# Kernel tuning notes

Measured on AMD Instinct MI355X. Metric: run time of the kernel, lower is better.

Reference implementation:

```python
import jax, jax.numpy as jnp
import numpy as np

N, F_IN, HID, HEADS, E, G, CLS = 20000, 128, 32, 8, 320000, 64, 10


def setup_inputs() -> dict:
    key = jax.random.key(0)
    ks = jax.random.split(key, 16)
    HC = HEADS * HID
    inp = {
        'x': jax.random.normal(ks[0], (N, F_IN), jnp.float32),
        'edge_index': jax.random.randint(ks[1], (2, E), 0, N, jnp.int64),
        'batch': jnp.sort(jax.random.randint(ks[2], (N,), 0, G, jnp.int64)),
        'W1': jax.random.normal(ks[3], (F_IN, HC), jnp.float32) * 0.1,
        'att_l1': jax.random.normal(ks[4], (HEADS, HID), jnp.float32) * 0.1,
        'att_r1': jax.random.normal(ks[5], (HEADS, HID), jnp.float32) * 0.1,
        'b1': jnp.zeros((HC,), jnp.float32),
        'W2': jax.random.normal(ks[6], (HC, HC), jnp.float32) * 0.1,
        'att_l2': jax.random.normal(ks[7], (HEADS, HID), jnp.float32) * 0.1,
        'att_r2': jax.random.normal(ks[8], (HEADS, HID), jnp.float32) * 0.1,
        'b2': jnp.zeros((HC,), jnp.float32),
        'lin_W': jax.random.normal(ks[9], (HC, CLS), jnp.float32) * 0.1,
        'lin_b': jnp.zeros((CLS,), jnp.float32),
    }
    return inp


def _add_self_loops(edge_index):
    loops = jnp.arange(N, dtype=edge_index.dtype)
    return (jnp.concatenate([edge_index[0], loops]),
            jnp.concatenate([edge_index[1], loops]))


def _supergat_conv(x, edge_index, W, att_l, att_r, b):
    # SuperGATConv, attention_type='MX', eval mode (no dropout / neg sampling)
    h = (x @ W).reshape(-1, HEADS, HID)          # [N, H, C]
    src, dst = _add_self_loops(edge_index)       # j -> i
    x_j = h[src]                                 # [Etot, H, C]
    x_i = h[dst]
    logits = jnp.einsum('ehc,ehc->eh', x_i, x_j)            # dot-product part
    alpha = jnp.einsum('ehc,hc->eh', x_j, att_l) + jnp.einsum('ehc,hc->eh', x_i, att_r)
    alpha = alpha * jax.nn.sigmoid(logits)
    alpha = jax.nn.leaky_relu(alpha, 0.2)
    # segment softmax over incoming edges of each dst node
    amax = jax.ops.segment_max(alpha, dst, num_segments=N)
    ex = jnp.exp(alpha - amax[dst])
    denom = jax.ops.segment_sum(ex, dst, num_segments=N)
    attn = ex / (denom[dst] + 1e-16)             # [Etot, H]
    out = jax.ops.segment_sum(x_j * attn[..., None], dst, num_segments=N)  # [N,H,C]
    return out.reshape(-1, HEADS * HID) + b


def reference(x, edge_index, batch, W1, att_l1, att_r1, b1, W2, att_l2, att_r2, b2, lin_W, lin_b):
    h = _supergat_conv(x, edge_index, W1, att_l1, att_r1, b1)
    h = jax.nn.elu(h)
    h = _supergat_conv(h, edge_index, W2, att_l2, att_r2, b2)
    # global mean pool over graphs
    sums = jax.ops.segment_sum(h, batch, num_segments=G)
    cnts = jax.ops.segment_sum(jnp.ones((h.shape[0], 1), h.dtype), batch, num_segments=G)
    pooled = sums / jnp.maximum(cnts, 1.0)
    return pooled @ lin_W + lin_b
```

## Files before the change

### kernel.cpp

```cpp
#include <hip/hip_runtime.h>
#include <hip/hip_bf16.h>
#include <math.h>

#define NNODE 20000
#define FIN   128
#define HC    256
#define HEADS 8
#define HID   32
#define NEDGE 320000
#define ETOT  (NEDGE + NNODE)
#define NGRAPH 64
#define NCLS  10
#define MAXDEG 64

typedef __attribute__((ext_vector_type(8))) short short8v;
typedef __attribute__((ext_vector_type(8))) unsigned short ushort8v;
typedef __attribute__((ext_vector_type(4))) float float4v;

__device__ __forceinline__ ushort f2bf(float f) {
    __hip_bfloat16 b = __float2bfloat16(f);
    return *(ushort*)&b;
}
__device__ __forceinline__ float bf2f(ushort u) {
    return __uint_as_float(((unsigned)u) << 16);
}


#define ZB_DEG ((NNODE + 255) / 256)
#define ZB_PS  ((NGRAPH * HC + NGRAPH + 255) / 256)

__global__ __launch_bounds__(256) void init_kernel(const float* __restrict__ W1,
                                                   const float* __restrict__ W2,
                                                   ushort* __restrict__ W1t,
                                                   ushort* __restrict__ W2t,
                                                   int* __restrict__ deg,
                                                   float* __restrict__ psum) {
    int b = blockIdx.x;
    if (b < 128) {
        int e = b * 256 + threadIdx.x;
        int k = e >> 8, n = e & 255;
        W1t[(long)n * FIN + k] = f2bf(W1[(long)k * 256 + n]);
    } else if (b < 384) {
        int e = (b - 128) * 256 + threadIdx.x;
        int k = e >> 8, n = e & 255;
        W2t[(long)n * HC + k] = f2bf(W2[(long)k * 256 + n]);
    } else if (b < 384 + ZB_DEG) {
        int i = (b - 384) * 256 + threadIdx.x;
        if (i < NNODE) deg[i] = 0;
    } else {
        int i = (b - 384 - ZB_DEG) * 256 + threadIdx.x;
        if (i < NGRAPH * HC + NGRAPH) psum[i] = 0.f;
    }
}


__global__ __launch_bounds__(256) void fill_slots(const int* __restrict__ ei,
                                                  int* __restrict__ deg,
                                                  int* __restrict__ esrc) {
    int e = blockIdx.x * blockDim.x + threadIdx.x;
    if (e >= ETOT) return;
    int src, dst;
    if (e < NEDGE) { src = ei[e]; dst = ei[NEDGE + e]; }
    else           { src = e - NEDGE; dst = src; }
    int slot = atomicAdd(&deg[dst], 1);
    if (slot < MAXDEG) esrc[dst * MAXDEG + slot] = src;
}


template<bool A_FP32>
__global__ __launch_bounds__(256) void gemm_mfma(const void* __restrict__ Aptr,
                                                 const ushort* __restrict__ Bt,
                                                 ushort* __restrict__ C,
                                                 const float* __restrict__ attL,
                                                 const float* __restrict__ attR,
                                                 float* __restrict__ aL,
                                                 float* __restrict__ aR,
                                                 int M, int K) {
    __shared__ __align__(16) ushort As[64][72];
    __shared__ __align__(16) ushort Bs[64][72];
    int tid = threadIdx.x;
    int rowBase = blockIdx.x * 64;
    int colBase = blockIdx.y * 64;
    int wave = tid >> 6;
    int l = tid & 63;
    int lm = l & 15;
    int quad = l >> 4;
    int r0 = (wave >> 1) * 32;
    int c0 = (wave & 1) * 32;

    float4v acc00 = {0.f, 0.f, 0.f, 0.f};
    float4v acc01 = acc00, acc10 = acc00, acc11 = acc00;

    for (int k0 = 0; k0 < K; k0 += 64) {
        if (A_FP32) {
            const float* A = (const float*)Aptr;
            #pragma unroll
            for (int q = 0; q < 4; q++) {
                int idx = tid + q * 256;
                int r   = idx >> 4;
                int kc  = (idx & 15) * 4;
                int grow = rowBase + r;
                float4 v = make_float4(0.f, 0.f, 0.f, 0.f);
                if (grow < M) v = *(const float4*)(A + (long)grow * K + k0 + kc);
                ushort4 o = { f2bf(v.x), f2bf(v.y), f2bf(v.z), f2bf(v.w) };
                *(ushort4*)&As[r][kc] = o;
            }
            #pragma unroll
            for (int q = 0; q < 2; q++) {
                int ch = tid + q * 256;
                int r  = ch >> 3;
                int kc = (ch & 7) * 8;
                *(short8v*)&Bs[r][kc] =
                    *(const short8v*)(Bt + (long)(colBase + r) * K + k0 + kc);
            }
        } else {
            const ushort* A = (const ushort*)Aptr;
            #pragma unroll
            for (int q = 0; q < 2; q++) {
                int ch = tid + q * 256;
                int r  = ch >> 3;
                int kc = (ch & 7) * 8;
                int grow = rowBase + r;
                short8v av = {};
                if (grow < M) av = *(const short8v*)(A + (long)grow * K + k0 + kc);
                *(short8v*)&As[r][kc] = av;
                *(short8v*)&Bs[r][kc] =
                    *(const short8v*)(Bt + (long)(colBase + r) * K + k0 + kc);
            }
        }
        __syncthreads();
        #pragma unroll
        for (int ks = 0; ks < 64; ks += 32) {
            int kb = ks + quad * 8;
            short8v a0 = *(const short8v*)&As[r0 + lm][kb];
            short8v a1 = *(const short8v*)&As[r0 + 16 + lm][kb];
            short8v b0 = *(const short8v*)&Bs[c0 + lm][kb];
            short8v b1 = *(const short8v*)&Bs[c0 + 16 + lm][kb];
            acc00 = __builtin_amdgcn_mfma_f32_16x16x32_bf16(a0, b0, acc00, 0, 0, 0);
            acc01 = __builtin_amdgcn_mfma_f32_16x16x32_bf16(a0, b1, acc01, 0, 0, 0);
            acc10 = __builtin_amdgcn_mfma_f32_16x16x32_bf16(a1, b0, acc10, 0, 0, 0);
            acc11 = __builtin_amdgcn_mfma_f32_16x16x32_bf16(a1, b1, acc11, 0, 0, 0);
        }
        __syncthreads();
    }

    int cb = colBase + c0;
    int hd = cb >> 5;
    float al0 = attL[cb + lm], al1 = attL[cb + 16 + lm];
    float ar0 = attR[cb + lm], ar1 = attR[cb + 16 + lm];
    #pragma unroll
    for (int mi = 0; mi < 2; mi++) {
        float4v s0 = mi ? acc10 : acc00;
        float4v s1 = mi ? acc11 : acc01;
        #pragma unroll
        for (int r = 0; r < 4; r++) {
            int row = rowBase + r0 + mi * 16 + quad * 4 + r;
            float pl = s0[r] * al0 + s1[r] * al1;
            float pr = s0[r] * ar0 + s1[r] * ar1;
            #pragma unroll
            for (int s2 = 1; s2 < 16; s2 <<= 1) {
                pl += __shfl_xor(pl, s2);
                pr += __shfl_xor(pr, s2);
            }
            if (row < M) {
                C[(long)row * 256 + cb + lm]      = f2bf(s0[r]);
                C[(long)row * 256 + cb + 16 + lm] = f2bf(s1[r]);
                if (lm == 0) {
                    aL[row * 8 + hd] = pl;
                    aR[row * 8 + hd] = pr;
                }
            }
        }
    }
}


__global__ __launch_bounds__(256) void fused_attn(const ushort* __restrict__ h,
                                                  const int* __restrict__ degv,
                                                  const int* __restrict__ esrc,
                                                  const float* __restrict__ aL,
                                                  const float* __restrict__ aR,
                                                  const float* __restrict__ bias,
                                                  ushort* __restrict__ out,
                                                  int apply_elu) {
    int wave = threadIdx.x >> 6;
    int node = blockIdx.x * 4 + wave;
    if (node >= NNODE) return;
    int l = threadIdx.x & 63;
    int slot = l >> 5;
    int lh = l & 31;
    int head = lh >> 2;

    const ushort8v* h8 = (const ushort8v*)h;
    ushort8v hiu = h8[(long)node * 32 + lh];
    float hi[8];
    #pragma unroll
    for (int c = 0; c < 8; c++) hi[c] = bf2f(hiu[c]);
    float a_ri = aR[node * 8 + head];
    int beg = node * MAXDEG;
    int deg = min(degv[node], MAXDEG);

    float lsum = 0.f;
    float acc[8] = {0.f, 0.f, 0.f, 0.f, 0.f, 0.f, 0.f, 0.f};

    int p  = slot;
    int j  = (p < deg)     ? esrc[beg + p]     : 0;
    int jn = (p + 2 < deg) ? esrc[beg + p + 2] : 0;
    for (; p < deg; p += 2) {
        ushort8v hju = h8[(long)j * 32 + lh];
        float a_lj = aL[j * 8 + head];
        j = jn;
        jn = (p + 4 < deg) ? esrc[beg + p + 4] : 0;
        float hj[8];
        #pragma unroll
        for (int c = 0; c < 8; c++) hj[c] = bf2f(hju[c]);
        float prod = hi[0] * hj[0];
        #pragma unroll
        for (int c = 1; c < 8; c++) prod += hi[c] * hj[c];
        prod += __shfl_xor(prod, 1);
        prod += __shfl_xor(prod, 2);
        float alpha = (a_lj + a_ri) * __builtin_amdgcn_rcpf(1.f + __expf(-prod));
        alpha = (alpha > 0.f) ? alpha : 0.2f * alpha;
        float ex = __expf(alpha);
        lsum += ex;
        #pragma unroll
        for (int c = 0; c < 8; c++) acc[c] += ex * hj[c];
    }

    lsum += __shfl_xor(lsum, 32);
    #pragma unroll
    for (int c = 0; c < 8; c++) acc[c] += __shfl_xor(acc[c], 32);

    if (slot == 0) {
        float inv = __builtin_amdgcn_rcpf(lsum + 1e-16f);
        float4 b0 = ((const float4*)bias)[lh * 2];
        float4 b1 = ((const float4*)bias)[lh * 2 + 1];
        float bb[8] = {b0.x, b0.y, b0.z, b0.w, b1.x, b1.y, b1.z, b1.w};
        ushort8v o;
        #pragma unroll
        for (int c = 0; c < 8; c++) {
            float r = acc[c] * inv + bb[c];
            if (apply_elu) r = (r > 0.f) ? r : (__expf(r) - 1.f);
            o[c] = f2bf(r);
        }
        *(ushort8v*)(out + (long)node * 256 + lh * 8) = o;
    }
}


__global__ __launch_bounds__(256) void pool_kernel(const ushort* __restrict__ h,
                                                   const int* __restrict__ batch,
                                                   float* __restrict__ psum,
                                                   float* __restrict__ pcnt) {
    int t = threadIdx.x;
    int n0 = blockIdx.x * 64;
    int n1 = min(n0 + 64, NNODE);
    if (n0 >= NNODE) return;
    float accv = 0.f;
    int gcur = batch[n0];
    for (int n = n0; n < n1; ++n) {
        int g = batch[n];
        if (g != gcur) {
            atomicAdd(&psum[gcur * HC + t], accv);
            accv = 0.f;
            gcur = g;
        }
        accv += bf2f(h[(long)n * HC + t]);
    }
    atomicAdd(&psum[gcur * HC + t], accv);
    if (t == 0) {
        int cnt = 0;
        int gc = batch[n0];
        for (int n = n0; n < n1; ++n) {
            int g = batch[n];
            if (g != gc) { atomicAdd(&pcnt[gc], (float)cnt); cnt = 0; gc = g; }
            cnt++;
        }
        atomicAdd(&pcnt[gc], (float)cnt);
    }
}

__global__ void final_kernel(const float* __restrict__ psum, const float* __restrict__ pcnt,
                             const float* __restrict__ linW, const float* __restrict__ linb,
                             float* __restrict__ out) {
    int g = blockIdx.x;
    int t = threadIdx.x;
    __shared__ float p[HC];
    float c = fmaxf(pcnt[g], 1.f);
    p[t] = psum[g * HC + t] / c;
    __syncthreads();
    if (t < NCLS) {
        float s = linb[t];
        for (int cch = 0; cch < HC; cch++) s += p[cch] * linW[cch * NCLS + t];
        out[g * NCLS + t] = s;
    }
}


extern "C" void kernel_launch(void* const* d_in, const int* in_sizes, int n_in,
                              void* d_out, int out_size, void* d_ws, size_t ws_size,
                              hipStream_t stream) {
    const float* x     = (const float*)d_in[0];
    const int*   ei    = (const int*)d_in[1];
    const int*   batch = (const int*)d_in[2];
    const float* W1    = (const float*)d_in[3];
    const float* attL1 = (const float*)d_in[4];
    const float* attR1 = (const float*)d_in[5];
    const float* b1    = (const float*)d_in[6];
    const float* W2    = (const float*)d_in[7];
    const float* attL2 = (const float*)d_in[8];
    const float* attR2 = (const float*)d_in[9];
    const float* b2    = (const float*)d_in[10];
    const float* linW  = (const float*)d_in[11];
    const float* linb  = (const float*)d_in[12];
    float* out = (float*)d_out;

    char* w = (char*)d_ws;
    size_t o = 0;
    int* deg    = (int*)(w + o); o += (size_t)NNODE * 4;
    o = (o + 15) & ~(size_t)15;
    int* esrc   = (int*)(w + o); o += (size_t)NNODE * MAXDEG * 4;
    o = (o + 15) & ~(size_t)15;
    ushort* W1t = (ushort*)(w + o); o += (size_t)FIN * HC * 2;
    ushort* W2t = (ushort*)(w + o); o += (size_t)HC * HC * 2;
    o = (o + 15) & ~(size_t)15;
    ushort* hbA = (ushort*)(w + o); o += (size_t)NNODE * HC * 2;
    ushort* hbB = (ushort*)(w + o); o += (size_t)NNODE * HC * 2;
    o = (o + 15) & ~(size_t)15;
    float* aL   = (float*)(w + o); o += (size_t)NNODE * HEADS * 4;
    float* aR   = (float*)(w + o); o += (size_t)NNODE * HEADS * 4;
    float* psum = (float*)(w + o); o += (size_t)NGRAPH * HC * 4;
    float* pcnt = (float*)(w + o); o += (size_t)NGRAPH * 4;

    init_kernel<<<384 + ZB_DEG + ZB_PS, 256, 0, stream>>>(W1, W2, W1t, W2t, deg, psum);

    int eb = (ETOT + 255) / 256;
    fill_slots<<<eb, 256, 0, stream>>>(ei, deg, esrc);

    dim3 gg((NNODE + 63) / 64, HC / 64);
    int ab = (NNODE + 3) / 4;
    gemm_mfma<true><<<gg, 256, 0, stream>>>(x, W1t, hbA, attL1, attR1, aL, aR, NNODE, FIN);
    fused_attn<<<ab, 256, 0, stream>>>(hbA, deg, esrc, aL, aR, b1, hbB, 1);
    gemm_mfma<false><<<gg, 256, 0, stream>>>(hbB, W2t, hbA, attL2, attR2, aL, aR, NNODE, HC);
    fused_attn<<<ab, 256, 0, stream>>>(hbA, deg, esrc, aL, aR, b2, hbB, 0);
    pool_kernel<<<(NNODE + 63) / 64, 256, 0, stream>>>(hbB, batch, psum, pcnt);
    final_kernel<<<NGRAPH, 256, 0, stream>>>(psum, pcnt, linW, linb, out);
}
```

Before: 219.9 us.

## Prefetch GEMM tiles, deepen attention gather pipeline, fuse pooling with classifier

The GEMM now loads the next K tile into registers while computing on the current shared-memory tile, overlapping global loads with MFMA work. The attention kernel prefetches neighbor features two edges ahead instead of one, to hide gather latency. Pooling and the final linear layer are merged into one kernel per graph that finds the graph's node range by binary search over the sorted batch array. This removes atomics, the psum zeroing and one launch, but runs only 64 blocks over the pooled data.

```diff
diff --git a/kernel.cpp b/kernel.cpp
--- a/kernel.cpp
+++ b/kernel.cpp
@@ -27,14 +27,12 @@
 
 
 #define ZB_DEG ((NNODE + 255) / 256)
-#define ZB_PS  ((NGRAPH * HC + NGRAPH + 255) / 256)
 
 __global__ __launch_bounds__(256) void init_kernel(const float* __restrict__ W1,
                                                    const float* __restrict__ W2,
                                                    ushort* __restrict__ W1t,
                                                    ushort* __restrict__ W2t,
-                                                   int* __restrict__ deg,
-                                                   float* __restrict__ psum) {
+                                                   int* __restrict__ deg) {
     int b = blockIdx.x;
     if (b < 128) {
         int e = b * 256 + threadIdx.x;
@@ -44,12 +42,9 @@
         int e = (b - 128) * 256 + threadIdx.x;
         int k = e >> 8, n = e & 255;
         W2t[(long)n * HC + k] = f2bf(W2[(long)k * 256 + n]);
-    } else if (b < 384 + ZB_DEG) {
+    } else {
         int i = (b - 384) * 256 + threadIdx.x;
         if (i < NNODE) deg[i] = 0;
-    } else {
-        int i = (b - 384 - ZB_DEG) * 256 + threadIdx.x;
-        if (i < NGRAPH * HC + NGRAPH) psum[i] = 0.f;
     }
 }
 
@@ -91,8 +86,12 @@
     float4v acc00 = {0.f, 0.f, 0.f, 0.f};
     float4v acc01 = acc00, acc10 = acc00, acc11 = acc00;
 
-    for (int k0 = 0; k0 < K; k0 += 64) {
-        if (A_FP32) {
+    float4  af[4];
+    short8v ab[2];
+    short8v bb[2];
+
+    auto load_tile = [&](int k0) {
+        if constexpr (A_FP32) {
             const float* A = (const float*)Aptr;
             #pragma unroll
             for (int q = 0; q < 4; q++) {
@@ -102,16 +101,7 @@
                 int grow = rowBase + r;
                 float4 v = make_float4(0.f, 0.f, 0.f, 0.f);
                 if (grow < M) v = *(const float4*)(A + (long)grow * K + k0 + kc);
-                ushort4 o = { f2bf(v.x), f2bf(v.y), f2bf(v.z), f2bf(v.w) };
-                *(ushort4*)&As[r][kc] = o;
-            }
-            #pragma unroll
-            for (int q = 0; q < 2; q++) {
-                int ch = tid + q * 256;
-                int r  = ch >> 3;
-                int kc = (ch & 7) * 8;
-                *(short8v*)&Bs[r][kc] =
-                    *(const short8v*)(Bt + (long)(colBase + r) * K + k0 + kc);
+                af[q] = v;
             }
         } else {
             const ushort* A = (const ushort*)Aptr;
@@ -123,12 +113,52 @@
                 int grow = rowBase + r;
                 short8v av = {};
                 if (grow < M) av = *(const short8v*)(A + (long)grow * K + k0 + kc);
-                *(short8v*)&As[r][kc] = av;
-                *(short8v*)&Bs[r][kc] =
-                    *(const short8v*)(Bt + (long)(colBase + r) * K + k0 + kc);
-            }
-        }
+                ab[q] = av;
+            }
+        }
+        #pragma unroll
+        for (int q = 0; q < 2; q++) {
+            int ch = tid + q * 256;
+            int r  = ch >> 3;
+            int kc = (ch & 7) * 8;
+            bb[q] = *(const short8v*)(Bt + (long)(colBase + r) * K + k0 + kc);
+        }
+    };
+
+    auto store_tile = [&]() {
+        if constexpr (A_FP32) {
+            #pragma unroll
+            for (int q = 0; q < 4; q++) {
+                int idx = tid + q * 256;
+                int r   = idx >> 4;
+                int kc  = (idx & 15) * 4;
+                float4 v = af[q];
+                ushort4 o = { f2bf(v.x), f2bf(v.y), f2bf(v.z), f2bf(v.w) };
+                *(ushort4*)&As[r][kc] = o;
+            }
+        } else {
+            #pragma unroll
+            for (int q = 0; q < 2; q++) {
+                int ch = tid + q * 256;
+                int r  = ch >> 3;
+                int kc = (ch & 7) * 8;
+                *(short8v*)&As[r][kc] = ab[q];
+            }
+        }
+        #pragma unroll
+        for (int q = 0; q < 2; q++) {
+            int ch = tid + q * 256;
+            int r  = ch >> 3;
+            int kc = (ch & 7) * 8;
+            *(short8v*)&Bs[r][kc] = bb[q];
+        }
+    };
+
+    load_tile(0);
+    for (int k0 = 0; k0 < K; k0 += 64) {
+        store_tile();
         __syncthreads();
+        if (k0 + 64 < K) load_tile(k0 + 64);
         #pragma unroll
         for (int ks = 0; ks < 64; ks += 32) {
             int kb = ks + quad * 8;
@@ -204,27 +234,37 @@
     float acc[8] = {0.f, 0.f, 0.f, 0.f, 0.f, 0.f, 0.f, 0.f};
 
     int p  = slot;
-    int j  = (p < deg)     ? esrc[beg + p]     : 0;
-    int jn = (p + 2 < deg) ? esrc[beg + p + 2] : 0;
+    int j0 = (p     < deg) ? esrc[beg + p]     : 0;
+    int j1 = (p + 2 < deg) ? esrc[beg + p + 2] : 0;
+    int j2 = (p + 4 < deg) ? esrc[beg + p + 4] : 0;
+    ushort8v hb0 = h8[(long)j0 * 32 + lh];
+    float    ab0 = aL[j0 * 8 + head];
+    ushort8v hb1 = h8[(long)j1 * 32 + lh];
+    float    ab1 = aL[j1 * 8 + head];
+
     for (; p < deg; p += 2) {
-        ushort8v hju = h8[(long)j * 32 + lh];
-        float a_lj = aL[j * 8 + head];
-        j = jn;
-        jn = (p + 4 < deg) ? esrc[beg + p + 4] : 0;
+        ushort8v hb2 = h8[(long)j2 * 32 + lh];
+        float    ab2 = aL[j2 * 8 + head];
+        int j3 = (p + 6 < deg) ? esrc[beg + p + 6] : 0;
+
         float hj[8];
         #pragma unroll
-        for (int c = 0; c < 8; c++) hj[c] = bf2f(hju[c]);
+        for (int c = 0; c < 8; c++) hj[c] = bf2f(hb0[c]);
         float prod = hi[0] * hj[0];
         #pragma unroll
         for (int c = 1; c < 8; c++) prod += hi[c] * hj[c];
         prod += __shfl_xor(prod, 1);
         prod += __shfl_xor(prod, 2);
-        float alpha = (a_lj + a_ri) * __builtin_amdgcn_rcpf(1.f + __expf(-prod));
+        float alpha = (ab0 + a_ri) * __builtin_amdgcn_rcpf(1.f + __expf(-prod));
         alpha = (alpha > 0.f) ? alpha : 0.2f * alpha;
         float ex = __expf(alpha);
         lsum += ex;
         #pragma unroll
         for (int c = 0; c < 8; c++) acc[c] += ex * hj[c];
+
+        hb0 = hb1; ab0 = ab1;
+        hb1 = hb2; ab1 = ab2;
+        j2  = j3;
     }
 
     lsum += __shfl_xor(lsum, 32);
@@ -248,51 +288,49 @@
 }
 
 
-__global__ __launch_bounds__(256) void pool_kernel(const ushort* __restrict__ h,
+__global__ __launch_bounds__(1024) void pool_final(const ushort* __restrict__ h,
                                                    const int* __restrict__ batch,
-                                                   float* __restrict__ psum,
-                                                   float* __restrict__ pcnt) {
-    int t = threadIdx.x;
-    int n0 = blockIdx.x * 64;
-    int n1 = min(n0 + 64, NNODE);
-    if (n0 >= NNODE) return;
-    float accv = 0.f;
-    int gcur = batch[n0];
-    for (int n = n0; n < n1; ++n) {
-        int g = batch[n];
-        if (g != gcur) {
-            atomicAdd(&psum[gcur * HC + t], accv);
-            accv = 0.f;
-            gcur = g;
-        }
-        accv += bf2f(h[(long)n * HC + t]);
-    }
-    atomicAdd(&psum[gcur * HC + t], accv);
-    if (t == 0) {
-        int cnt = 0;
-        int gc = batch[n0];
-        for (int n = n0; n < n1; ++n) {
-            int g = batch[n];
-            if (g != gc) { atomicAdd(&pcnt[gc], (float)cnt); cnt = 0; gc = g; }
-            cnt++;
-        }
-        atomicAdd(&pcnt[gc], (float)cnt);
-    }
-}
-
-__global__ void final_kernel(const float* __restrict__ psum, const float* __restrict__ pcnt,
-                             const float* __restrict__ linW, const float* __restrict__ linb,
-                             float* __restrict__ out) {
+                                                   const float* __restrict__ linW,
+                                                   const float* __restrict__ linb,
+                                                   float* __restrict__ out) {
     int g = blockIdx.x;
     int t = threadIdx.x;
-    __shared__ float p[HC];
-    float c = fmaxf(pcnt[g], 1.f);
-    p[t] = psum[g * HC + t] / c;
+
+    int lo = 0, hb = NNODE;
+    while (lo < hb) { int mid = (lo + hb) >> 1; if (batch[mid] < g) lo = mid + 1; else hb = mid; }
+    int s = lo;
+    lo = 0; hb = NNODE;
+    while (lo < hb) { int mid = (lo + hb) >> 1; if (batch[mid] < g + 1) lo = mid + 1; else hb = mid; }
+    int e = lo;
+
+    int r  = t >> 5;
+    int ch = (t & 31) * 8;
+    float acc[8] = {0.f, 0.f, 0.f, 0.f, 0.f, 0.f, 0.f, 0.f};
+    for (int n = s + r; n < e; n += 32) {
+        ushort8v v = *(const ushort8v*)(h + (long)n * 256 + ch);
+        #pragma unroll
+        for (int c = 0; c < 8; c++) acc[c] += bf2f(v[c]);
+    }
+
+    __shared__ float red[32][256];
+    #pragma unroll
+    for (int c = 0; c < 8; c++) red[r][ch + c] = acc[c];
     __syncthreads();
+
+    __shared__ float pooled[256];
+    if (t < 256) {
+        float sum = 0.f;
+        #pragma unroll
+        for (int r2 = 0; r2 < 32; r2++) sum += red[r2][t];
+        float cnt = fmaxf((float)(e - s), 1.f);
+        pooled[t] = sum / cnt;
+    }
+    __syncthreads();
+
     if (t < NCLS) {
-        float s = linb[t];
-        for (int cch = 0; cch < HC; cch++) s += p[cch] * linW[cch * NCLS + t];
-        out[g * NCLS + t] = s;
+        float o = linb[t];
+        for (int c = 0; c < HC; c++) o += pooled[c] * linW[c * NCLS + t];
+        out[g * NCLS + t] = o;
     }
 }
 
@@ -329,10 +367,8 @@
     o = (o + 15) & ~(size_t)15;
     float* aL   = (float*)(w + o); o += (size_t)NNODE * HEADS * 4;
     float* aR   = (float*)(w + o); o += (size_t)NNODE * HEADS * 4;
-    float* psum = (float*)(w + o); o += (size_t)NGRAPH * HC * 4;
-    float* pcnt = (float*)(w + o); o += (size_t)NGRAPH * 4;
-
-    init_kernel<<<384 + ZB_DEG + ZB_PS, 256, 0, stream>>>(W1, W2, W1t, W2t, deg, psum);
+
+    init_kernel<<<384 + ZB_DEG, 256, 0, stream>>>(W1, W2, W1t, W2t, deg);
 
     int eb = (ETOT + 255) / 256;
     fill_slots<<<eb, 256, 0, stream>>>(ei, deg, esrc);
@@ -343,6 +379,5 @@
     fused_attn<<<ab, 256, 0, stream>>>(hbA, deg, esrc, aL, aR, b1, hbB, 1);
     gemm_mfma<false><<<gg, 256, 0, stream>>>(hbB, W2t, hbA, attL2, attR2, aL, aR, NNODE, HC);
     fused_attn<<<ab, 256, 0, stream>>>(hbA, deg, esrc, aL, aR, b2, hbB, 0);
-    pool_kernel<<<(NNODE + 63) / 64, 256, 0, stream>>>(hbB, batch, psum, pcnt);
-    final_kernel<<<NGRAPH, 256, 0, stream>>>(psum, pcnt, linW, linb, out);
-}
+    pool_final<<<NGRAPH, 1024, 0, stream>>>(hbB, batch, linW, linb, out);
+}
```

Result: faster. 206.6 us (-6.0%).
